# Kernel tuning notes

Hardware: AMD Instinct MI355X
Metric: run time of the kernel (lower is better)

## Reference

```python
import jax, jax.numpy as jnp
import numpy as np

D, BEV_H, BEV_W, NH, NP = 256, 200, 200, 8, 8
NQ = BEV_H * BEV_W
DFF = 1024
HD = D // NH


def setup_inputs() -> dict:
    key = jax.random.key(0)
    ks = jax.random.split(key, 12)
    def rn(k, shape, scale=0.02):
        return jax.random.normal(k, shape, jnp.float32) * scale
    return dict(
        B_adj0=rn(ks[0], (1, NQ, D), 1.0),
        B_adj1=rn(ks[1], (1, NQ, D), 1.0),
        query_embed=rn(ks[2], (NQ, D), 1.0),
        W_ref=rn(ks[3], (D, 2)), b_ref=jnp.zeros((2,), jnp.float32),
        W_off=rn(ks[4], (D, NH * NP * 2)), b_off=rn(ks[5], (NH * NP * 2,), 0.5),
        W_attn=rn(ks[6], (D, NH * NP)), b_attn=jnp.zeros((NH * NP,), jnp.float32),
        W_val=rn(ks[7], (D, D)), b_val=jnp.zeros((D,), jnp.float32),
        W_out=rn(ks[8], (D, D)), b_out=jnp.zeros((D,), jnp.float32),
        W_ffn1=rn(ks[9], (D, DFF)), b_ffn1=jnp.zeros((DFF,), jnp.float32),
        W_ffn2=rn(ks[10], (DFF, D)), b_ffn2=jnp.zeros((D,), jnp.float32),
    )


def _deform_attend(value, loc, attn_w):
    """Bilinear-sample `value` (bs,NQ,NH,HD laid out as BEV_H x BEV_W map) at
    normalized locations loc (bs,nq,NH,NP,2) with align_corners=False and zero
    padding (torch grid_sample semantics), weighted by attn_w (bs,nq,NH,NP)."""
    bs, _, nh, hd = value.shape
    nq = loc.shape[1]
    vt = value.transpose(0, 2, 1, 3)  # (bs, nh, HW, hd)
    # grid = 2*loc - 1 ; pixel = ((grid+1)*size - 1)/2 = loc*size - 0.5
    x = loc[..., 0] * BEV_W - 0.5
    y = loc[..., 1] * BEV_H - 0.5
    x0f = jnp.floor(x); y0f = jnp.floor(y)
    lx = x - x0f; ly = y - y0f
    x0 = x0f.astype(jnp.int32); y0 = y0f.astype(jnp.int32)
    acc = jnp.zeros((bs, nh, nq, hd), value.dtype)
    corners = ((0, 0, (1 - lx) * (1 - ly)), (1, 0, lx * (1 - ly)),
               (0, 1, (1 - lx) * ly), (1, 1, lx * ly))
    for dx, dy, w in corners:
        ix = x0 + dx
        iy = y0 + dy
        valid = ((ix >= 0) & (ix < BEV_W) & (iy >= 0) & (iy < BEV_H)).astype(value.dtype)
        idx = jnp.clip(iy, 0, BEV_H - 1) * BEV_W + jnp.clip(ix, 0, BEV_W - 1)  # (bs,nq,nh,np)
        idx_t = idx.transpose(0, 2, 1, 3).reshape(bs, nh, nq * NP)
        v = jnp.take_along_axis(vt, idx_t[..., None], axis=2).reshape(bs, nh, nq, NP, hd)
        wt = (w * valid * attn_w).transpose(0, 2, 1, 3)  # (bs,nh,nq,np)
        acc = acc + (wt[..., None] * v).sum(3)
    return acc.transpose(0, 2, 1, 3).reshape(bs, nq, nh * hd)


def reference(B_adj0, B_adj1, query_embed, W_ref, b_ref, W_off, b_off,
              W_attn, b_attn, W_val, b_val, W_out, b_out,
              W_ffn1, b_ffn1, W_ffn2, b_ffn2):
    bs = B_adj0.shape[0]
    q = jnp.broadcast_to(query_embed[None], (bs, NQ, D))
    # reference points in [0,1]
    ref = jax.nn.sigmoid(q @ W_ref + b_ref)  # (bs,nq,2)
    off = (q @ W_off + b_off).reshape(bs, NQ, NH, NP, 2)
    attn = jax.nn.softmax((q @ W_attn + b_attn).reshape(bs, NQ, NH, NP), axis=-1)
    offset_normalizer = jnp.array([BEV_W, BEV_H], jnp.float32)
    loc = ref[:, :, None, None, :] + off / offset_normalizer  # (bs,nq,nh,np,2)
    B_short = jnp.zeros((bs, NQ, D), B_adj0.dtype)
    for V in (B_adj0, B_adj1):
        val = (V @ W_val + b_val).reshape(bs, NQ, NH, HD)
        out = _deform_attend(val, loc, attn) @ W_out + b_out
        B_short = B_short + out + q  # mmcv MSDA residual: identity = query
    # FFN with residual (mmcv FFN, add_identity=True, drop=0)
    ffn = jax.nn.relu(B_short @ W_ffn1 + b_ffn1) @ W_ffn2 + b_ffn2
    return B_short + ffn
```

## Files before the change

kernel.cpp:

```cpp
#include <hip/hip_runtime.h>
#include <hip/hip_bf16.h>

#define NQ    40000
#define DD    256
#define NHH   8
#define NPP   8
#define DFF   1024
#define BEV   200
#define MPAD  40064

typedef __attribute__((ext_vector_type(4))) float f32x4;
typedef __attribute__((ext_vector_type(8))) short s16x8;
typedef __hip_bfloat16 bf16;

#define AS1(p) ((const __attribute__((address_space(1))) void*)(p))
#define AS3(p) ((__attribute__((address_space(3))) void*)(p))

__device__ inline unsigned short f2bf(float f) {
  union { bf16 h; unsigned short u; } cv;
  cv.h = __float2bfloat16(f);
  return cv.u;
}
__device__ inline float bf2f(bf16 h) { return __bfloat162float(h); }
__device__ inline float bfs(short u) {
  union { float f; unsigned u; } c;
  c.u = ((unsigned)(unsigned short)u) << 16;
  return c.f;
}

__global__ void transpose_cvt(const float* __restrict__ src, bf16* __restrict__ dst,
                              int R, int C) {
  int i = blockIdx.x * 256 + threadIdx.x;
  if (i >= R * C) return;
  int c = i / R, r = i % R;
  dst[i] = __float2bfloat16(src[(size_t)r * C + c]);
}

__global__ void build_wq(const float* __restrict__ Woff, const float* __restrict__ Wattn,
                         const float* __restrict__ Wref, bf16* __restrict__ dst) {
  int i = blockIdx.x * 256 + threadIdx.x;
  int n = i >> 8, k = i & 255;
  float v;
  if (n < 128)      v = Woff[k * 128 + n];
  else if (n < 192) v = Wattn[k * 64 + (n - 128)];
  else if (n < 194) v = Wref[k * 2 + (n - 192)];
  else              v = 0.f;
  dst[i] = __float2bfloat16(v);
}

__global__ void cvt_both_kernel(const float* __restrict__ qe,
                                const float* __restrict__ a, const float* __restrict__ b,
                                bf16* __restrict__ qeb, bf16* __restrict__ vsum, int n4) {
  int i = blockIdx.x * 256 + threadIdx.x;
  if (i >= n4) return;
  float4 q4 = ((const float4*)qe)[i];
  ushort4 oq;
  oq.x = f2bf(q4.x); oq.y = f2bf(q4.y); oq.z = f2bf(q4.z); oq.w = f2bf(q4.w);
  ((ushort4*)qeb)[i] = oq;
  float4 va = ((const float4*)a)[i];
  float4 vb = ((const float4*)b)[i];
  ushort4 o;
  o.x = f2bf(va.x + vb.x); o.y = f2bf(va.y + vb.y);
  o.z = f2bf(va.z + vb.z); o.w = f2bf(va.w + vb.w);
  ((ushort4*)vsum)[i] = o;
}

template<int BK_, bool RELU>
__global__ void gemm_bt(const bf16* __restrict__ A, const bf16* __restrict__ Bt,
                        int K, int Ntiles, int N,
                        const float* __restrict__ bias, float biasScale,
                        const bf16* __restrict__ addB, float addScale,
                        bf16* __restrict__ outB, float* __restrict__ outF, int Mvalid) {
  constexpr int HALF = BK_ * 256;
  constexpr int ROWB = BK_ * 2;
  constexpr int BUFB = BK_ * 512;
  __shared__ __align__(16) char smem[2 * BUFB];
  const int tid  = threadIdx.x;
  const int wave = tid >> 6, lane = tid & 63;
  const int nwg = gridDim.x;
  const int orig = blockIdx.x;
  const int q8 = nwg >> 3, r8 = nwg & 7;
  const int xcd = orig & 7, idx = orig >> 3;
  const int wg = (xcd < r8 ? xcd * (q8 + 1) : r8 * (q8 + 1) + (xcd - r8) * q8) + idx;
  const int tm = wg / Ntiles, tn = wg % Ntiles;
  const int wr = wave >> 1, wc = wave & 1;

  f32x4 acc[4][4];
#pragma unroll
  for (int i = 0; i < 4; ++i)
#pragma unroll
    for (int j = 0; j < 4; ++j) {
      f32x4 z = {0.f, 0.f, 0.f, 0.f};
      acc[i][j] = z;
    }

  const char* Ab = (const char*)A;
  const char* Bb = (const char*)Bt;
  const int nK = K / BK_;

  auto stage = [&](int bufBase, int kt) {
    constexpr int WI = BK_ / 8;
#pragma unroll
    for (int i = 0; i < WI; ++i) {
      const int j  = wave * WI + i;
      const int p0 = j << 10;
      const char* g;
      if (p0 < HALF) {
        const int pl = p0 + lane * 16;
        const int row = pl / ROWB, cb = pl % ROWB;
        g = Ab + ((size_t)(tm * 128 + row) * K + kt * BK_) * 2 + cb;
      } else {
        const int pl = p0 - HALF + lane * 16;
        const int row = pl / ROWB, cb = pl % ROWB;
        g = Bb + ((size_t)(tn * 128 + row) * K + kt * BK_) * 2 + cb;
      }
      __builtin_amdgcn_global_load_lds(AS1(g), AS3(smem + bufBase + p0), 16, 0, 0);
    }
  };

  stage(0, 0);
  __syncthreads();
  int cur = 0;
  for (int kt = 0; kt < nK; ++kt) {
    if (kt + 1 < nK) stage((cur ^ 1) * BUFB, kt + 1);
    const char* sbuf = smem + cur * BUFB;
    constexpr int NKK = BK_ / 32;
#pragma unroll
    for (int kk = 0; kk < NKK; ++kk) {
      const int r  = lane & 15;
      const int kb = kk * 64 + (lane >> 4) * 16;
      s16x8 af[4], bfr[4];
#pragma unroll
      for (int mr = 0; mr < 4; ++mr)
        af[mr] = *(const s16x8*)(sbuf + (wr * 64 + mr * 16 + r) * ROWB + kb);
#pragma unroll
      for (int nr = 0; nr < 4; ++nr)
        bfr[nr] = *(const s16x8*)(sbuf + HALF + (wc * 64 + nr * 16 + r) * ROWB + kb);
#pragma unroll
      for (int mr = 0; mr < 4; ++mr)
#pragma unroll
        for (int nr = 0; nr < 4; ++nr)
          acc[mr][nr] = __builtin_amdgcn_mfma_f32_16x16x32_bf16(af[mr], bfr[nr], acc[mr][nr], 0, 0, 0);
    }
    __syncthreads();
    cur ^= 1;
  }

  const int r = lane & 15, rg = lane >> 4;
#pragma unroll
  for (int mr = 0; mr < 4; ++mr) {
#pragma unroll
    for (int nr = 0; nr < 4; ++nr) {
      const int gn = tn * 128 + wc * 64 + nr * 16 + r;
      const float bval = bias ? biasScale * bias[gn] : 0.f;
#pragma unroll
      for (int j2 = 0; j2 < 4; ++j2) {
        const int gm = tm * 128 + wr * 64 + mr * 16 + rg * 4 + j2;
        float v = acc[mr][nr][j2] + bval;
        if (addB && gm < Mvalid) v += addScale * bf2f(addB[(size_t)gm * N + gn]);
        if (RELU) v = fmaxf(v, 0.f);
        if (outB) outB[(size_t)gm * N + gn] = __float2bfloat16(v);
        if (outF && gm < Mvalid) outF[(size_t)gm * N + gn] = v;
      }
    }
  }
}

__global__ __launch_bounds__(256)
void fused_ffn(const bf16* __restrict__ Bsh, const bf16* __restrict__ Wf1t,
               const bf16* __restrict__ Wf2t,
               const float* __restrict__ b1, const float* __restrict__ b2,
               float* __restrict__ outF, int Mvalid) {
  constexpr int BUFB = 20480;
  __shared__ __align__(16) char smem[2 * BUFB];
  __shared__ __align__(16) char hbuf[64 * 544];
  const int tid  = threadIdx.x;
  const int wave = tid >> 6, lane = tid & 63;
  const int r = lane & 15, hi = lane >> 4;
  const int nwg = gridDim.x;
  const int orig = blockIdx.x;
  const int q8 = nwg >> 3, r8_ = nwg & 7;
  const int xcd = orig & 7, idx = orig >> 3;
  const int tm = (xcd < r8_ ? xcd * (q8 + 1) : r8_ * (q8 + 1) + (xcd - r8_) * q8) + idx;

  f32x4 acc[4][4];
#pragma unroll
  for (int i = 0; i < 4; ++i)
#pragma unroll
    for (int j = 0; j < 4; ++j) {
      f32x4 z = {0.f, 0.f, 0.f, 0.f};
      acc[i][j] = z;
    }

  const char* Ab = (const char*)Bsh;
  const char* W1 = (const char*)Wf1t;
  const char* W2 = (const char*)Wf2t;

  auto stage1 = [&](int bufBase, int chunk, int kt) {
#pragma unroll
    for (int i = 0; i < 5; ++i) {
      const int p0 = (wave * 5 + i) << 10;
      const char* g;
      if (p0 < 4096) {
        const int pl = p0 + lane * 16;
        const int row = pl >> 6, cb = pl & 63;
        g = Ab + ((size_t)(tm * 64 + row) * 256 + kt * 32) * 2 + cb;
      } else {
        const int pl = p0 - 4096 + lane * 16;
        const int row = pl >> 6, cb = pl & 63;
        g = W1 + ((size_t)(chunk * 256 + row) * 256 + kt * 32) * 2 + cb;
      }
      __builtin_amdgcn_global_load_lds(AS1(g), AS3(smem + bufBase + p0), 16, 0, 0);
    }
  };
  auto stage2 = [&](int bufBase, int chunk, int kt) {
#pragma unroll
    for (int i = 0; i < 4; ++i) {
      const int p0 = (wave * 4 + i) << 10;
      const int pl = p0 + lane * 16;
      const int row = pl >> 6, cb = pl & 63;
      const char* g = W2 + ((size_t)row * 1024 + chunk * 256 + kt * 32) * 2 + cb;
      __builtin_amdgcn_global_load_lds(AS1(g), AS3(smem + bufBase + p0), 16, 0, 0);
    }
  };

  for (int chunk = 0; chunk < 4; ++chunk) {
    f32x4 acc_h[4][4];
#pragma unroll
    for (int i = 0; i < 4; ++i)
#pragma unroll
      for (int j = 0; j < 4; ++j) {
        f32x4 z = {0.f, 0.f, 0.f, 0.f};
        acc_h[i][j] = z;
      }
    stage1(0, chunk, 0);
    __syncthreads();
    int cur = 0;
    for (int kt = 0; kt < 8; ++kt) {
      if (kt + 1 < 8) stage1((cur ^ 1) * BUFB, chunk, kt + 1);
      const char* sbuf = smem + cur * BUFB;
      const int kb = hi * 16;
      s16x8 af[4], bfr[4];
#pragma unroll
      for (int mr = 0; mr < 4; ++mr)
        af[mr] = *(const s16x8*)(sbuf + (mr * 16 + r) * 64 + kb);
#pragma unroll
      for (int nr = 0; nr < 4; ++nr)
        bfr[nr] = *(const s16x8*)(sbuf + 4096 + (wave * 64 + nr * 16 + r) * 64 + kb);
#pragma unroll
      for (int mr = 0; mr < 4; ++mr)
#pragma unroll
        for (int nr = 0; nr < 4; ++nr)
          acc_h[mr][nr] = __builtin_amdgcn_mfma_f32_16x16x32_bf16(af[mr], bfr[nr], acc_h[mr][nr], 0, 0, 0);
      __syncthreads();
      cur ^= 1;
    }
#pragma unroll
    for (int nr = 0; nr < 4; ++nr) {
      const int hcol = wave * 64 + nr * 16 + r;
      const float bv = b1[chunk * 256 + hcol];
#pragma unroll
      for (int mr = 0; mr < 4; ++mr)
#pragma unroll
        for (int j2 = 0; j2 < 4; ++j2) {
          const int row = mr * 16 + hi * 4 + j2;
          const float v = fmaxf(acc_h[mr][nr][j2] + bv, 0.f);
          *(unsigned short*)(hbuf + row * 544 + hcol * 2) = f2bf(v);
        }
    }
    __syncthreads();
    stage2(0, chunk, 0);
    __syncthreads();
    cur = 0;
    for (int kt = 0; kt < 8; ++kt) {
      if (kt + 1 < 8) stage2((cur ^ 1) * BUFB, chunk, kt + 1);
      const char* sbuf = smem + cur * BUFB;
      const int kb = hi * 16;
      s16x8 af[4], bfr[4];
#pragma unroll
      for (int mr = 0; mr < 4; ++mr)
        af[mr] = *(const s16x8*)(hbuf + (mr * 16 + r) * 544 + kt * 64 + kb);
#pragma unroll
      for (int nr = 0; nr < 4; ++nr)
        bfr[nr] = *(const s16x8*)(sbuf + (wave * 64 + nr * 16 + r) * 64 + kb);
#pragma unroll
      for (int mr = 0; mr < 4; ++mr)
#pragma unroll
        for (int nr = 0; nr < 4; ++nr)
          acc[mr][nr] = __builtin_amdgcn_mfma_f32_16x16x32_bf16(af[mr], bfr[nr], acc[mr][nr], 0, 0, 0);
      __syncthreads();
      cur ^= 1;
    }
    __syncthreads();
  }

#pragma unroll
  for (int mr = 0; mr < 4; ++mr) {
#pragma unroll
    for (int nr = 0; nr < 4; ++nr) {
      const int gn = wave * 64 + nr * 16 + r;
      const float bval = b2[gn];
#pragma unroll
      for (int j2 = 0; j2 < 4; ++j2) {
        const int gm = tm * 64 + mr * 16 + hi * 4 + j2;
        if (gm < Mvalid) {
          float v = acc[mr][nr][j2] + bval + bf2f(Bsh[(size_t)gm * 256 + gn]);
          outF[(size_t)gm * 256 + gn] = v;
        }
      }
    }
  }
}

__global__ void finalize_kernel(const bf16* __restrict__ raw, const float* __restrict__ b_off,
                                const float* __restrict__ b_attn, const float* __restrict__ b_ref,
                                float* __restrict__ samp) {
  __shared__ float r[4][256];
  const int tid = threadIdx.x;
  const int q0 = blockIdx.x * 4;
#pragma unroll
  for (int i = 0; i < 4; ++i) {
    int e = tid + i * 256;
    int ql = e >> 8, k = e & 255;
    r[ql][k] = bf2f(raw[(size_t)(q0 + ql) * 256 + k]);
  }
  __syncthreads();
  const int ql = tid >> 6, hp = tid & 63;
  const int h = hp >> 3, p = hp & 7;
  float v[8];
  float m = -1e30f;
#pragma unroll
  for (int pp = 0; pp < 8; ++pp) {
    v[pp] = r[ql][128 + h * 8 + pp] + b_attn[h * 8 + pp];
    m = fmaxf(m, v[pp]);
  }
  float s = 0.f;
#pragma unroll
  for (int pp = 0; pp < 8; ++pp) { v[pp] = expf(v[pp] - m); s += v[pp]; }
  const float w = v[p] / s;
  const float sx = 1.f / (1.f + expf(-(r[ql][192] + b_ref[0])));
  const float sy = 1.f / (1.f + expf(-(r[ql][193] + b_ref[1])));
  const float px = sx * (float)BEV + (r[ql][hp * 2 + 0] + b_off[hp * 2 + 0]) - 0.5f;
  const float py = sy * (float)BEV + (r[ql][hp * 2 + 1] + b_off[hp * 2 + 1]) - 0.5f;
  const size_t o = ((size_t)(q0 + ql) * 64 + hp) * 3;
  samp[o] = px; samp[o + 1] = py; samp[o + 2] = w;
}

__global__ __launch_bounds__(256, 4)
void deform_kernel(const float* __restrict__ samp, const bf16* __restrict__ val,
                   bf16* __restrict__ out) {
  __shared__ float s[8 * 192];
  const int tid = threadIdx.x;
  const int q0 = blockIdx.x * 8;
#pragma unroll
  for (int i = 0; i < 6; ++i) {
    const int e = tid + i * 256;
    s[e] = samp[(size_t)q0 * 192 + e];
  }
  __syncthreads();
  const int ql = tid >> 5;
  const int lane5 = tid & 31;
  const int h = lane5 >> 2;
  const int dg = lane5 & 3;
  const float* sp = s + ql * 192 + h * 24;
  const bf16* vb = val + h * 32 + dg * 8;

  float acc[8] = {0.f, 0.f, 0.f, 0.f, 0.f, 0.f, 0.f, 0.f};
#pragma unroll 2
  for (int p = 0; p < 8; ++p) {
    const float px = sp[p * 3 + 0], py = sp[p * 3 + 1], w = sp[p * 3 + 2];
    const float xf = floorf(px), yf = floorf(py);
    const int x0 = (int)xf, y0 = (int)yf;
    const float lx = px - xf, ly = py - yf;
    const float xa = (x0 >= 0 && x0 < BEV) ? 1.f : 0.f;
    const float xb = (x0 + 1 >= 0 && x0 + 1 < BEV) ? 1.f : 0.f;
    const float ya = (y0 >= 0 && y0 < BEV) ? 1.f : 0.f;
    const float yb = (y0 + 1 >= 0 && y0 + 1 < BEV) ? 1.f : 0.f;
    const float w00 = w * (1.f - lx) * (1.f - ly) * xa * ya;
    const float w10 = w * lx * (1.f - ly) * xb * ya;
    const float w01 = w * (1.f - lx) * ly * xa * yb;
    const float w11 = w * lx * ly * xb * yb;
    const int cx0 = min(max(x0, 0), BEV - 1);
    const int cx1 = min(max(x0 + 1, 0), BEV - 1);
    const int cy0 = min(max(y0, 0), BEV - 1) * BEV;
    const int cy1 = min(max(y0 + 1, 0), BEV - 1) * BEV;
    const s16x8 v00 = *(const s16x8*)(vb + (size_t)(cy0 + cx0) * 256);
    const s16x8 v10 = *(const s16x8*)(vb + (size_t)(cy0 + cx1) * 256);
    const s16x8 v01 = *(const s16x8*)(vb + (size_t)(cy1 + cx0) * 256);
    const s16x8 v11 = *(const s16x8*)(vb + (size_t)(cy1 + cx1) * 256);
#pragma unroll
    for (int j = 0; j < 8; ++j) {
      acc[j] += w00 * bfs(v00[j]) + w10 * bfs(v10[j])
              + w01 * bfs(v01[j]) + w11 * bfs(v11[j]);
    }
  }
  s16x8 o;
#pragma unroll
  for (int j = 0; j < 8; ++j) o[j] = (short)f2bf(acc[j]);
  *(s16x8*)(out + (size_t)(q0 + ql) * 256 + h * 32 + dg * 8) = o;
}

extern "C" void kernel_launch(void* const* d_in, const int* in_sizes, int n_in,
                              void* d_out, int out_size, void* d_ws, size_t ws_size,
                              hipStream_t stream) {
  const float* B0     = (const float*)d_in[0];
  const float* B1     = (const float*)d_in[1];
  const float* qe     = (const float*)d_in[2];
  const float* W_ref  = (const float*)d_in[3];
  const float* b_ref  = (const float*)d_in[4];
  const float* W_off  = (const float*)d_in[5];
  const float* b_off  = (const float*)d_in[6];
  const float* W_attn = (const float*)d_in[7];
  const float* b_attn = (const float*)d_in[8];
  const float* W_val  = (const float*)d_in[9];
  const float* b_val  = (const float*)d_in[10];
  const float* W_out  = (const float*)d_in[11];
  const float* b_out  = (const float*)d_in[12];
  const float* W_ffn1 = (const float*)d_in[13];
  const float* b_ffn1 = (const float*)d_in[14];
  const float* W_ffn2 = (const float*)d_in[15];
  const float* b_ffn2 = (const float*)d_in[16];
  float* out = (float*)d_out;
  char* ws = (char*)d_ws;

  const size_t SZ_MAT = (size_t)MPAD * 256 * 2;
  const size_t VAL_OFF    = 0;
  const size_t RAW_OFF    = SZ_MAT;
  const size_t BSH_OFF    = 2 * SZ_MAT;
  const size_t QE_OFF     = 3 * SZ_MAT;
  const size_t VSUM_OFF   = 4 * SZ_MAT;
  const size_t SAMP_OFF   = 5 * SZ_MAT;
  const size_t SAMP_BYTES = (size_t)NQ * 192 * 4;
  const size_t WQ_OFF     = SAMP_OFF + SAMP_BYTES;
  const size_t WVAL_OFF   = WQ_OFF   + 256 * 256 * 2;
  const size_t WOUT_OFF   = WVAL_OFF + 256 * 256 * 2;
  const size_t WF1_OFF    = WOUT_OFF + 256 * 256 * 2;
  const size_t WF2_OFF    = WF1_OFF  + 1024 * 256 * 2;

  bf16* valb  = (bf16*)(ws + VAL_OFF);
  bf16* rawb  = (bf16*)(ws + RAW_OFF);
  bf16* defb  = rawb;
  bf16* bshb  = (bf16*)(ws + BSH_OFF);
  bf16* qeb   = (bf16*)(ws + QE_OFF);
  bf16* vsum  = (bf16*)(ws + VSUM_OFF);
  float* samp = (float*)(ws + SAMP_OFF);
  bf16* wq    = (bf16*)(ws + WQ_OFF);
  bf16* wval  = (bf16*)(ws + WVAL_OFF);
  bf16* wout  = (bf16*)(ws + WOUT_OFF);
  bf16* wf1   = (bf16*)(ws + WF1_OFF);
  bf16* wf2   = (bf16*)(ws + WF2_OFF);

  const int n4 = NQ * 256 / 4;
  const int MT64 = MPAD / 64;
  const int MT128 = MPAD / 128;

  build_wq<<<256, 256, 0, stream>>>(W_off, W_attn, W_ref, wq);
  transpose_cvt<<<(256 * 256 + 255) / 256, 256, 0, stream>>>(W_val, wval, 256, 256);
  transpose_cvt<<<(256 * 256 + 255) / 256, 256, 0, stream>>>(W_out, wout, 256, 256);
  transpose_cvt<<<(256 * 1024 + 255) / 256, 256, 0, stream>>>(W_ffn1, wf1, 256, 1024);
  transpose_cvt<<<(1024 * 256 + 255) / 256, 256, 0, stream>>>(W_ffn2, wf2, 1024, 256);

  cvt_both_kernel<<<n4 / 256, 256, 0, stream>>>(qe, B0, B1, qeb, vsum, n4);

  gemm_bt<32, false><<<MT128 * 2, 256, 0, stream>>>(qeb, wq, 256, 2, 256,
                                                    nullptr, 0.f, nullptr, 0.f,
                                                    rawb, nullptr, NQ);
  finalize_kernel<<<NQ / 4, 256, 0, stream>>>(rawb, b_off, b_attn, b_ref, samp);

  gemm_bt<32, false><<<MT128 * 2, 256, 0, stream>>>(vsum, wval, 256, 2, 256,
                                                    b_val, 2.f, nullptr, 0.f,
                                                    valb, nullptr, NQ);

  deform_kernel<<<NQ / 8, 256, 0, stream>>>(samp, valb, defb);

  gemm_bt<32, false><<<MT128 * 2, 256, 0, stream>>>(defb, wout, 256, 2, 256,
                                                    b_out, 2.f, qeb, 2.f,
                                                    bshb, nullptr, NQ);

  fused_ffn<<<MT64, 256, 0, stream>>>(bshb, wf1, wf2, b_ffn1, b_ffn2, out, NQ);
}
```

Baseline: 269.1 us.

## Shrink fused FFN hidden chunk to 128 and read A directly from global

```diff
diff --git a/kernel.cpp b/kernel.cpp
--- a/kernel.cpp
+++ b/kernel.cpp
@@ -171,9 +171,8 @@
                const bf16* __restrict__ Wf2t,
                const float* __restrict__ b1, const float* __restrict__ b2,
                float* __restrict__ outF, int Mvalid) {
-  constexpr int BUFB = 20480;
-  __shared__ __align__(16) char smem[2 * BUFB];
-  __shared__ __align__(16) char hbuf[64 * 544];
+  __shared__ __align__(16) char wbuf[2][16384];
+  __shared__ __align__(16) char hbuf[64 * 272];
   const int tid  = threadIdx.x;
   const int wave = tid >> 6, lane = tid & 63;
   const int r = lane & 15, hi = lane >> 4;
@@ -192,97 +191,86 @@
       acc[i][j] = z;
     }
 
-  const char* Ab = (const char*)Bsh;
+  const bf16* Arow = Bsh + (size_t)(tm * 64) * 256;
   const char* W1 = (const char*)Wf1t;
   const char* W2 = (const char*)Wf2t;
 
-  auto stage1 = [&](int bufBase, int chunk, int kt) {
-#pragma unroll
-    for (int i = 0; i < 5; ++i) {
-      const int p0 = (wave * 5 + i) << 10;
-      const char* g;
-      if (p0 < 4096) {
-        const int pl = p0 + lane * 16;
-        const int row = pl >> 6, cb = pl & 63;
-        g = Ab + ((size_t)(tm * 64 + row) * 256 + kt * 32) * 2 + cb;
-      } else {
-        const int pl = p0 - 4096 + lane * 16;
-        const int row = pl >> 6, cb = pl & 63;
-        g = W1 + ((size_t)(chunk * 256 + row) * 256 + kt * 32) * 2 + cb;
-      }
-      __builtin_amdgcn_global_load_lds(AS1(g), AS3(smem + bufBase + p0), 16, 0, 0);
+  auto stage1 = [&](int buf, int c, int kt) {
+#pragma unroll
+    for (int i = 0; i < 2; ++i) {
+      const int p0 = (wave * 2 + i) << 10;
+      const int pl = p0 + lane * 16;
+      const int row = pl >> 6, cb = pl & 63;
+      const char* g = W1 + ((size_t)(c * 128 + row) * 256 + kt * 32) * 2 + cb;
+      __builtin_amdgcn_global_load_lds(AS1(g), AS3(&wbuf[buf][p0]), 16, 0, 0);
     }
   };
-  auto stage2 = [&](int bufBase, int chunk, int kt) {
+  auto stage2 = [&](int buf, int c, int kt) {
 #pragma unroll
     for (int i = 0; i < 4; ++i) {
       const int p0 = (wave * 4 + i) << 10;
       const int pl = p0 + lane * 16;
       const int row = pl >> 6, cb = pl & 63;
-      const char* g = W2 + ((size_t)row * 1024 + chunk * 256 + kt * 32) * 2 + cb;
-      __builtin_amdgcn_global_load_lds(AS1(g), AS3(smem + bufBase + p0), 16, 0, 0);
+      const char* g = W2 + ((size_t)row * 1024 + c * 128 + kt * 32) * 2 + cb;
+      __builtin_amdgcn_global_load_lds(AS1(g), AS3(&wbuf[buf][p0]), 16, 0, 0);
     }
   };
 
-  for (int chunk = 0; chunk < 4; ++chunk) {
-    f32x4 acc_h[4][4];
+  for (int c = 0; c < 8; ++c) {
+    f32x4 acc_h[4][2];
 #pragma unroll
     for (int i = 0; i < 4; ++i)
 #pragma unroll
-      for (int j = 0; j < 4; ++j) {
+      for (int j = 0; j < 2; ++j) {
         f32x4 z = {0.f, 0.f, 0.f, 0.f};
         acc_h[i][j] = z;
       }
-    stage1(0, chunk, 0);
+    stage1(0, c, 0);
     __syncthreads();
     int cur = 0;
     for (int kt = 0; kt < 8; ++kt) {
-      if (kt + 1 < 8) stage1((cur ^ 1) * BUFB, chunk, kt + 1);
-      const char* sbuf = smem + cur * BUFB;
-      const int kb = hi * 16;
-      s16x8 af[4], bfr[4];
-#pragma unroll
-      for (int mr = 0; mr < 4; ++mr)
-        af[mr] = *(const s16x8*)(sbuf + (mr * 16 + r) * 64 + kb);
-#pragma unroll
-      for (int nr = 0; nr < 4; ++nr)
-        bfr[nr] = *(const s16x8*)(sbuf + 4096 + (wave * 64 + nr * 16 + r) * 64 + kb);
-#pragma unroll
-      for (int mr = 0; mr < 4; ++mr)
-#pragma unroll
-        for (int nr = 0; nr < 4; ++nr)
+      if (kt + 1 < 8) stage1(cur ^ 1, c, kt + 1);
+      s16x8 af[4], bfr[2];
+#pragma unroll
+      for (int mr = 0; mr < 4; ++mr)
+        af[mr] = *(const s16x8*)(Arow + (size_t)(mr * 16 + r) * 256 + kt * 32 + hi * 8);
+#pragma unroll
+      for (int nr = 0; nr < 2; ++nr)
+        bfr[nr] = *(const s16x8*)(&wbuf[cur][(wave * 32 + nr * 16 + r) * 64 + hi * 16]);
+#pragma unroll
+      for (int mr = 0; mr < 4; ++mr)
+#pragma unroll
+        for (int nr = 0; nr < 2; ++nr)
           acc_h[mr][nr] = __builtin_amdgcn_mfma_f32_16x16x32_bf16(af[mr], bfr[nr], acc_h[mr][nr], 0, 0, 0);
       __syncthreads();
       cur ^= 1;
     }
 #pragma unroll
-    for (int nr = 0; nr < 4; ++nr) {
-      const int hcol = wave * 64 + nr * 16 + r;
-      const float bv = b1[chunk * 256 + hcol];
+    for (int nr = 0; nr < 2; ++nr) {
+      const int hc = wave * 32 + nr * 16 + r;
+      const float bv = b1[c * 128 + hc];
 #pragma unroll
       for (int mr = 0; mr < 4; ++mr)
 #pragma unroll
         for (int j2 = 0; j2 < 4; ++j2) {
           const int row = mr * 16 + hi * 4 + j2;
-          const float v = fmaxf(acc_h[mr][nr][j2] + bv, 0.f);
-          *(unsigned short*)(hbuf + row * 544 + hcol * 2) = f2bf(v);
+          *(unsigned short*)(hbuf + row * 272 + hc * 2) =
+              f2bf(fmaxf(acc_h[mr][nr][j2] + bv, 0.f));
         }
     }
     __syncthreads();
-    stage2(0, chunk, 0);
+    stage2(0, c, 0);
     __syncthreads();
     cur = 0;
-    for (int kt = 0; kt < 8; ++kt) {
-      if (kt + 1 < 8) stage2((cur ^ 1) * BUFB, chunk, kt + 1);
-      const char* sbuf = smem + cur * BUFB;
-      const int kb = hi * 16;
+    for (int kt = 0; kt < 4; ++kt) {
+      if (kt + 1 < 4) stage2(cur ^ 1, c, kt + 1);
       s16x8 af[4], bfr[4];
 #pragma unroll
       for (int mr = 0; mr < 4; ++mr)
-        af[mr] = *(const s16x8*)(hbuf + (mr * 16 + r) * 544 + kt * 64 + kb);
+        af[mr] = *(const s16x8*)(hbuf + (mr * 16 + r) * 272 + (kt * 32 + hi * 8) * 2);
 #pragma unroll
       for (int nr = 0; nr < 4; ++nr)
-        bfr[nr] = *(const s16x8*)(sbuf + (wave * 64 + nr * 16 + r) * 64 + kb);
+        bfr[nr] = *(const s16x8*)(&wbuf[cur][(wave * 64 + nr * 16 + r) * 64 + hi * 16]);
 #pragma unroll
       for (int mr = 0; mr < 4; ++mr)
 #pragma unroll
@@ -291,7 +279,6 @@
       __syncthreads();
       cur ^= 1;
     }
-    __syncthreads();
   }
 
 #pragma unroll
@@ -304,8 +291,8 @@
       for (int j2 = 0; j2 < 4; ++j2) {
         const int gm = tm * 64 + mr * 16 + hi * 4 + j2;
         if (gm < Mvalid) {
-          float v = acc[mr][nr][j2] + bval + bf2f(Bsh[(size_t)gm * 256 + gn]);
-          outF[(size_t)gm * 256 + gn] = v;
+          outF[(size_t)gm * 256 + gn] =
+              acc[mr][nr][j2] + bval + bf2f(Bsh[(size_t)gm * 256 + gn]);
         }
       }
     }
```

Result: slower. 327.7 us (+21.8%).
